# Performance work log

Hardware: AMD Instinct MI355X
Metric: run time of the kernel (lower is better)

## Reference

```python
import jax, jax.numpy as jnp
import numpy as np

HEADS = 12
EMBED = 768
HEAD_DIM = EMBED // HEADS
SCALING = HEAD_DIM ** (-0.5)


def setup_inputs() -> dict:
    key = jax.random.key(0)
    k1, k2, k3, k4, k5 = jax.random.split(key, 5)
    B, N = 8, 1024
    x = jax.random.normal(k1, (B, N, EMBED), dtype=jnp.float32)
    W_qkv = jax.random.normal(k2, (3 * EMBED, EMBED), dtype=jnp.float32) * 0.02
    b_qkv = jax.random.normal(k3, (3 * EMBED,), dtype=jnp.float32) * 0.02
    W_proj = jax.random.normal(k4, (EMBED, EMBED), dtype=jnp.float32) * 0.02
    b_proj = jax.random.normal(k5, (EMBED,), dtype=jnp.float32) * 0.02
    return {"x": x, "W_qkv": W_qkv, "b_qkv": b_qkv, "W_proj": W_proj, "b_proj": b_proj}


def reference(x, W_qkv, b_qkv, W_proj, b_proj):
    B, N, D = x.shape
    # fused QKV projection: [B, N, 3D]
    qkv = x @ W_qkv.T + b_qkv
    # split last dim as (u=3, h, e) per einops 'b n (u h e) -> u b h n e'
    qkv = qkv.reshape(B, N, 3, HEADS, HEAD_DIM).transpose(2, 0, 3, 1, 4)
    q, k, v = qkv[0], qkv[1], qkv[2]
    # raw dot-product scores (NO pre-softmax scaling, per original)
    sim = jnp.einsum('bhqi,bhki->bhqk', q, k)
    # unusual POST-softmax scaling
    sim = jax.nn.softmax(sim, axis=-1) * SCALING
    att = jnp.einsum('bhnk,bhke->bhne', sim, v)
    att = att.transpose(0, 2, 1, 3).reshape(B, N, D)  # b h n e -> b n (h e)
    return att @ W_proj.T + b_proj
```

## Files before the change

### kernel.cpp

```cpp
#include <hip/hip_runtime.h>

typedef unsigned short u16;
typedef __attribute__((ext_vector_type(8))) short bf16x8;
typedef __attribute__((ext_vector_type(4))) float f32x4;

#define HEADS 12
#define HDIM  64
#define EMBED 768
#define TD    2304
#define SEQ   1024
#define MTOK  8192
#define GK    768
#define GNT   12

__device__ __forceinline__ u16 f2bf(float f) {
  union { float f; unsigned u; } x; x.f = f;
  unsigned r = x.u + 0x7fffu + ((x.u >> 16) & 1u);
  return (u16)(r >> 16);
}

__global__ void cast3_kernel(const float* __restrict__ x, const float* __restrict__ wq,
                             const float* __restrict__ wp, u16* __restrict__ xb,
                             u16* __restrict__ wqb, u16* __restrict__ wpb) {
  const int N1 = MTOK * EMBED / 4, N2 = TD * EMBED / 4, N3 = EMBED * EMBED / 4;
  int i = blockIdx.x * blockDim.x + threadIdx.x;
  int st = gridDim.x * blockDim.x;
  for (; i < N1 + N2 + N3; i += st) {
    const float* s; u16* d; int j;
    if (i < N1)           { s = x;  d = xb;  j = i; }
    else if (i < N1 + N2) { s = wq; d = wqb; j = i - N1; }
    else                  { s = wp; d = wpb; j = i - N1 - N2; }
    float4 v = reinterpret_cast<const float4*>(s)[j];
    ushort4 o;
    o.x = f2bf(v.x); o.y = f2bf(v.y); o.z = f2bf(v.z); o.w = f2bf(v.w);
    reinterpret_cast<ushort4*>(d)[j] = o;
  }
}

__device__ __forceinline__ void gload_lds16(const u16* g, u16* l) {
  __builtin_amdgcn_global_load_lds(
      (const __attribute__((address_space(1))) unsigned*)g,
      (__attribute__((address_space(3))) unsigned*)l, 16, 0, 0);
}

__device__ __forceinline__ void memfence_bar() {
  asm volatile("" ::: "memory");
  __builtin_amdgcn_s_barrier();
  asm volatile("" ::: "memory");
}

template <bool OUT_BF16>
__global__ __launch_bounds__(256, 2) void gemm_phase(const u16* __restrict__ A,
                                                     const u16* __restrict__ B,
                                                     const float* __restrict__ bias,
                                                     void* __restrict__ Cv,
                                                     int NBN, int Ndim) {
  __shared__ u16 As[3][128 * 64];
  __shared__ u16 Bs[2][96 * 64];
  const int tid  = threadIdx.x;
  const int wave = tid >> 6, lane = tid & 63;
  const int wr = wave >> 1, wc = wave & 1;
  const int lr = lane & 15, g = lane >> 4;

  const int nwg = gridDim.x;
  const int swz = (blockIdx.x & 7) * (nwg >> 3) + (blockIdx.x >> 3);
  const int ny = swz % NBN, mx = swz / NBN;

  const u16* Ag = A + (size_t)(mx * 128) * GK;
  const u16* Bg = B + (size_t)(ny * 96) * GK;

  const int srow   = lane >> 3;
  const int schunk = (lane & 7) ^ srow;

  auto stageA = [&](int kt, int buf) {
#pragma unroll
    for (int c = 0; c < 4; ++c) {
      int slot = wave * 4 + c;
      int row  = slot * 8 + srow;
      gload_lds16(Ag + (size_t)row * GK + kt * 64 + schunk * 8, &As[buf][slot * 512]);
    }
  };
  auto stageB = [&](int kt, int buf) {
#pragma unroll
    for (int c = 0; c < 3; ++c) {
      int slot = wave * 3 + c;
      int row  = slot * 8 + srow;
      gload_lds16(Bg + (size_t)row * GK + kt * 64 + schunk * 8, &Bs[buf][slot * 512]);
    }
  };

  f32x4 acc[4][3];
#pragma unroll
  for (int m = 0; m < 4; ++m)
#pragma unroll
    for (int n = 0; n < 3; ++n) acc[m][n] = 0.f;

  stageA(0, 0);
  stageB(0, 0);
  stageA(1, 1);
  asm volatile("s_waitcnt vmcnt(4)" ::: "memory");
  memfence_bar();

  int ra = 0, rb = 0;
  for (int t = 0; t < GNT; ++t) {
    bf16x8 af[4][2], bf0[3], bf1[3];
#pragma unroll
    for (int m = 0; m < 4; ++m)
#pragma unroll
      for (int kk = 0; kk < 2; ++kk) {
        int r = wr * 64 + m * 16 + lr;
        af[m][kk] = *reinterpret_cast<const bf16x8*>(
            &As[ra][r * 64 + (((kk * 4 + g) ^ (r & 7)) << 3)]);
      }
#pragma unroll
    for (int n = 0; n < 3; ++n) {
      int r = wc * 48 + n * 16 + lr;
      bf0[n] = *reinterpret_cast<const bf16x8*>(&Bs[rb][r * 64 + ((g ^ (r & 7)) << 3)]);
    }
    if (t + 1 < GNT) stageB(t + 1, rb ^ 1);
    if (t + 2 < GNT) stageA(t + 2, ra >= 1 ? ra - 1 : 2);
    memfence_bar();
    asm volatile("s_waitcnt lgkmcnt(0)" ::: "memory");
    __builtin_amdgcn_sched_barrier(0);
    __builtin_amdgcn_s_setprio(1);
#pragma unroll
    for (int m = 0; m < 4; ++m)
#pragma unroll
      for (int n = 0; n < 3; ++n)
        acc[m][n] = __builtin_amdgcn_mfma_f32_16x16x32_bf16(bf0[n], af[m][0], acc[m][n], 0, 0, 0);
    __builtin_amdgcn_s_setprio(0);

#pragma unroll
    for (int n = 0; n < 3; ++n) {
      int r = wc * 48 + n * 16 + lr;
      bf1[n] = *reinterpret_cast<const bf16x8*>(&Bs[rb][r * 64 + (((4 + g) ^ (r & 7)) << 3)]);
    }
    memfence_bar();
    asm volatile("s_waitcnt lgkmcnt(0)" ::: "memory");
    __builtin_amdgcn_sched_barrier(0);
    __builtin_amdgcn_s_setprio(1);
#pragma unroll
    for (int m = 0; m < 4; ++m)
#pragma unroll
      for (int n = 0; n < 3; ++n)
        acc[m][n] = __builtin_amdgcn_mfma_f32_16x16x32_bf16(bf1[n], af[m][1], acc[m][n], 0, 0, 0);
    __builtin_amdgcn_s_setprio(0);

    if (t < GNT - 2) {
      asm volatile("s_waitcnt vmcnt(4)" ::: "memory");
      memfence_bar();
    } else if (t == GNT - 2) {
      asm volatile("s_waitcnt vmcnt(0)" ::: "memory");
      memfence_bar();
    }
    ra = (ra == 2) ? 0 : ra + 1;
    rb ^= 1;
  }

  const int row0 = mx * 128 + wr * 64 + lr;
  const int col0 = ny * 96 + wc * 48 + g * 4;
#pragma unroll
  for (int m = 0; m < 4; ++m)
#pragma unroll
    for (int n = 0; n < 3; ++n) {
      int row = row0 + m * 16;
      int col = col0 + n * 16;
      float4 bv = *reinterpret_cast<const float4*>(&bias[col]);
      float v0 = acc[m][n][0] + bv.x, v1 = acc[m][n][1] + bv.y;
      float v2 = acc[m][n][2] + bv.z, v3 = acc[m][n][3] + bv.w;
      if (OUT_BF16) {
        ushort4 pw;
        pw.x = f2bf(v0); pw.y = f2bf(v1); pw.z = f2bf(v2); pw.w = f2bf(v3);
        *reinterpret_cast<ushort4*>(&((u16*)Cv)[(size_t)row * Ndim + col]) = pw;
      } else {
        *reinterpret_cast<float4*>(&((float*)Cv)[(size_t)row * Ndim + col]) =
            make_float4(v0, v1, v2, v3);
      }
    }
}

__global__ __launch_bounds__(256) void vtrans_kernel(const u16* __restrict__ qkv,
                                                     u16* __restrict__ vt) {
  const int bh = blockIdx.x, kb = blockIdx.y;
  const int b = bh / HEADS, h = bh % HEADS;
  __shared__ u16 Ls[64 * 72];
  const int t = threadIdx.x;
  const int row = t >> 2, seg = t & 3;
  const u16* src = qkv + (size_t)(b * SEQ + kb * 64 + row) * TD + 2 * EMBED + h * HDIM + seg * 16;
  *reinterpret_cast<uint4*>(&Ls[row * 72 + seg * 16])     = *reinterpret_cast<const uint4*>(src);
  *reinterpret_cast<uint4*>(&Ls[row * 72 + seg * 16 + 8]) = *reinterpret_cast<const uint4*>(src + 8);
  __syncthreads();
  u16 tmp[16];
#pragma unroll
  for (int i = 0; i < 16; ++i) tmp[i] = Ls[(seg * 16 + i) * 72 + row];
  u16* dst = vt + (size_t)bh * (HDIM * SEQ) + (size_t)row * SEQ + kb * 64 + seg * 16;
  *reinterpret_cast<uint4*>(dst)     = *reinterpret_cast<const uint4*>(tmp);
  *reinterpret_cast<uint4*>(dst + 8) = *reinterpret_cast<const uint4*>(tmp + 8);
}

__global__ __launch_bounds__(256, 3) void attn_kernel(const u16* __restrict__ qkv,
                                                      const u16* __restrict__ vt,
                                                      u16* __restrict__ ctx) {
  const int bh = blockIdx.x;
  const int b = bh / HEADS, h = bh % HEADS;
  const int qt = blockIdx.y;
  const int tid = threadIdx.x, wave = tid >> 6, lane = tid & 63;
  const int lr = lane & 15, g = lane >> 4;

  __shared__ u16 Ks[2][64 * 64];
  __shared__ u16 Vs[2][64 * 64];
  __shared__ u16 Ps[128 * 64];

  const size_t tok0 = (size_t)b * SEQ;
  const int q0 = qt * 128;
  const int mbase = wave * 32;

  bf16x8 qf[2][2];
#pragma unroll
  for (int mi = 0; mi < 2; ++mi)
#pragma unroll
    for (int dk = 0; dk < 2; ++dk)
      qf[mi][dk] = *reinterpret_cast<const bf16x8*>(
          qkv + (tok0 + q0 + mbase + mi * 16 + lr) * TD + h * HDIM + dk * 32 + g * 8);

  const int srow = lane >> 3;
  const int schunk = (lane & 7) ^ srow;
  const u16* vbase = vt + (size_t)bh * (HDIM * SEQ);

  auto stage = [&](int kb, int buf) {
#pragma unroll
    for (int c2 = 0; c2 < 2; ++c2) {
      int call = wave * 2 + c2;
      int row  = call * 8 + srow;
      gload_lds16(qkv + (tok0 + kb * 64 + row) * TD + EMBED + h * HDIM + schunk * 8,
                  &Ks[buf][call * 512]);
      gload_lds16(vbase + (size_t)row * SEQ + kb * 64 + schunk * 8,
                  &Vs[buf][call * 512]);
    }
  };

  f32x4 oacc[2][4];
#pragma unroll
  for (int mi = 0; mi < 2; ++mi)
#pragma unroll
    for (int e = 0; e < 4; ++e) oacc[mi][e] = 0.f;
  float psum[2] = {0.f, 0.f};

  stage(0, 0);
  asm volatile("s_waitcnt vmcnt(0)" ::: "memory");
  memfence_bar();

  int cur = 0;
  for (int kb = 0; kb < 16; ++kb) {
    if (kb < 15) stage(kb + 1, cur ^ 1);

    bf16x8 ka[4][2];
#pragma unroll
    for (int n = 0; n < 4; ++n)
#pragma unroll
      for (int dk = 0; dk < 2; ++dk) {
        int r = n * 16 + lr;
        int c = dk * 4 + g;
        ka[n][dk] = *reinterpret_cast<const bf16x8*>(&Ks[cur][r * 64 + ((c ^ (r & 7)) << 3)]);
      }
#pragma unroll
    for (int mi = 0; mi < 2; ++mi) {
      int m = mbase + mi * 16 + lr;
      int pswz = (lr & 7) << 1;
#pragma unroll
      for (int n = 0; n < 4; ++n) {
        f32x4 s = 0.f;
        __builtin_amdgcn_s_setprio(1);
        s = __builtin_amdgcn_mfma_f32_16x16x32_bf16(ka[n][0], qf[mi][0], s, 0, 0, 0);
        s = __builtin_amdgcn_mfma_f32_16x16x32_bf16(ka[n][1], qf[mi][1], s, 0, 0, 0);
        __builtin_amdgcn_s_setprio(0);
        float e0 = __expf(s[0]), e1 = __expf(s[1]);
        float e2 = __expf(s[2]), e3 = __expf(s[3]);
        psum[mi] += (e0 + e1) + (e2 + e3);
        ushort4 pw;
        pw.x = f2bf(e0); pw.y = f2bf(e1); pw.z = f2bf(e2); pw.w = f2bf(e3);
        int gran = n * 4 + g;
        *reinterpret_cast<ushort4*>(&Ps[m * 64 + ((gran ^ pswz) << 2)]) = pw;
      }
    }

    bf16x8 vb2[4][2];
#pragma unroll
    for (int e = 0; e < 4; ++e)
#pragma unroll
      for (int kk = 0; kk < 2; ++kk) {
        int r = e * 16 + lr;
        int c = kk * 4 + g;
        vb2[e][kk] = *reinterpret_cast<const bf16x8*>(&Vs[cur][r * 64 + ((c ^ (r & 7)) << 3)]);
      }
#pragma unroll
    for (int mi = 0; mi < 2; ++mi) {
      bf16x8 pa[2];
#pragma unroll
      for (int kk = 0; kk < 2; ++kk) {
        int r = mbase + mi * 16 + lr;
        int c = kk * 4 + g;
        pa[kk] = *reinterpret_cast<const bf16x8*>(&Ps[r * 64 + ((c ^ (r & 7)) << 3)]);
      }
      __builtin_amdgcn_s_setprio(1);
#pragma unroll
      for (int e = 0; e < 4; ++e) {
        oacc[mi][e] = __builtin_amdgcn_mfma_f32_16x16x32_bf16(pa[0], vb2[e][0], oacc[mi][e], 0, 0, 0);
        oacc[mi][e] = __builtin_amdgcn_mfma_f32_16x16x32_bf16(pa[1], vb2[e][1], oacc[mi][e], 0, 0, 0);
      }
      __builtin_amdgcn_s_setprio(0);
    }

    if (kb < 15) {
      asm volatile("s_waitcnt vmcnt(0)" ::: "memory");
      memfence_bar();
    }
    cur ^= 1;
  }

  float scl[2][4];
#pragma unroll
  for (int mi = 0; mi < 2; ++mi) {
    float v = psum[mi];
    v += __shfl_xor(v, 16);
    v += __shfl_xor(v, 32);
    v = 0.125f / v;
#pragma unroll
    for (int j = 0; j < 4; ++j) scl[mi][j] = __shfl(v, 4 * g + j);
  }
#pragma unroll
  for (int mi = 0; mi < 2; ++mi)
#pragma unroll
    for (int e = 0; e < 4; ++e)
#pragma unroll
      for (int j = 0; j < 4; ++j) {
        float v = oacc[mi][e][j] * scl[mi][j];
        ctx[(tok0 + q0 + mbase + mi * 16 + 4 * g + j) * EMBED + h * HDIM + e * 16 + lr] = f2bf(v);
      }
}

extern "C" void kernel_launch(void* const* d_in, const int* in_sizes, int n_in,
                              void* d_out, int out_size, void* d_ws, size_t ws_size,
                              hipStream_t stream) {
  (void)in_sizes; (void)n_in; (void)out_size;
  const float* x     = (const float*)d_in[0];
  const float* Wqkv  = (const float*)d_in[1];
  const float* bqkv  = (const float*)d_in[2];
  const float* Wproj = (const float*)d_in[3];
  const float* bproj = (const float*)d_in[4];
  float* out = (float*)d_out;

  char* ws = (char*)d_ws;
  size_t off = 0;
  auto alloc = [&](size_t bytes) {
    char* p = ws + off;
    off += (bytes + 255) & ~(size_t)255;
    return p;
  };
  u16* xb     = (u16*)alloc((size_t)MTOK * EMBED * 2);
  u16* wqkvb  = (u16*)alloc((size_t)TD * EMBED * 2);
  u16* wprojb = (u16*)alloc((size_t)EMBED * EMBED * 2);
  u16* qkvb   = (u16*)alloc((size_t)MTOK * TD * 2);
  u16* ctxb   = (u16*)alloc((size_t)MTOK * EMBED * 2);
  if (off > ws_size) return;
  u16* vtb = xb;

  cast3_kernel<<<dim3(2048), dim3(256), 0, stream>>>(x, Wqkv, Wproj, xb, wqkvb, wprojb);

  gemm_phase<true><<<dim3(1536), dim3(256), 0, stream>>>(xb, wqkvb, bqkv, qkvb, 24, TD);
  vtrans_kernel<<<dim3(96, 16), dim3(256), 0, stream>>>(qkvb, vtb);
  attn_kernel<<<dim3(96, 8), dim3(256), 0, stream>>>(qkvb, vtb, ctxb);
  gemm_phase<false><<<dim3(512), dim3(256), 0, stream>>>(ctxb, wprojb, bproj, out, 8, EMBED);
}
```

Measured before the change: 125.1 us.

## Restructure GEMM into triple-buffered K=32 pipeline with register double-buffering

The GEMM kernel now uses a K-step of 32 instead of 64, with triple-buffered LDS tiles for both A and B. Global loads are issued three stages ahead, and fragment reads for the next step are double-buffered in registers so they overlap the current MFMAs. The smaller LDS footprint allows launch bounds of 3 blocks per CU, but the XOR swizzle is dropped, which may bring LDS bank conflicts. In the attention kernel the V fragment loads are hoisted alongside the K loads, which raises register pressure.

Result: slower. 134.3 us (+7.3%).

```diff
diff --git a/kernel.cpp b/kernel.cpp
--- a/kernel.cpp
+++ b/kernel.cpp
@@ -11,7 +11,7 @@
 #define SEQ   1024
 #define MTOK  8192
 #define GK    768
-#define GNT   12
+#define GNT   24
 
 __device__ __forceinline__ u16 f2bf(float f) {
   union { float f; unsigned u; } x; x.f = f;
@@ -50,13 +50,13 @@
 }
 
 template <bool OUT_BF16>
-__global__ __launch_bounds__(256, 2) void gemm_phase(const u16* __restrict__ A,
-                                                     const u16* __restrict__ B,
-                                                     const float* __restrict__ bias,
-                                                     void* __restrict__ Cv,
-                                                     int NBN, int Ndim) {
-  __shared__ u16 As[3][128 * 64];
-  __shared__ u16 Bs[2][96 * 64];
+__global__ __launch_bounds__(256, 3) void gemm_pipe(const u16* __restrict__ A,
+                                                    const u16* __restrict__ B,
+                                                    const float* __restrict__ bias,
+                                                    void* __restrict__ Cv,
+                                                    int NBN, int Ndim) {
+  __shared__ u16 As[3][128 * 32];
+  __shared__ u16 Bs[3][96 * 32];
   const int tid  = threadIdx.x;
   const int wave = tid >> 6, lane = tid & 63;
   const int wr = wave >> 1, wc = wave & 1;
@@ -69,24 +69,38 @@
   const u16* Ag = A + (size_t)(mx * 128) * GK;
   const u16* Bg = B + (size_t)(ny * 96) * GK;
 
-  const int srow   = lane >> 3;
-  const int schunk = (lane & 7) ^ srow;
-
-  auto stageA = [&](int kt, int buf) {
-#pragma unroll
-    for (int c = 0; c < 4; ++c) {
-      int slot = wave * 4 + c;
-      int row  = slot * 8 + srow;
-      gload_lds16(Ag + (size_t)row * GK + kt * 64 + schunk * 8, &As[buf][slot * 512]);
-    }
-  };
-  auto stageB = [&](int kt, int buf) {
-#pragma unroll
-    for (int c = 0; c < 3; ++c) {
-      int slot = wave * 3 + c;
-      int row  = slot * 8 + srow;
-      gload_lds16(Bg + (size_t)row * GK + kt * 64 + schunk * 8, &Bs[buf][slot * 512]);
-    }
+  const int srow = lane >> 2;
+  const int scol = (lane & 3) * 8;
+
+  auto stage = [&](int kt) {
+    const int buf = kt % 3;
+    const int k0 = kt * 32;
+#pragma unroll
+    for (int c = 0; c < 2; ++c) {
+      int slot = wave * 2 + c;
+      int row  = slot * 16 + srow;
+      gload_lds16(Ag + (size_t)row * GK + k0 + scol, &As[buf][slot * 512]);
+    }
+    if (wave < 2) {
+#pragma unroll
+      for (int c = 0; c < 2; ++c) {
+        int slot = wave * 2 + c;
+        int row  = slot * 16 + srow;
+        gload_lds16(Bg + (size_t)row * GK + k0 + scol, &Bs[buf][slot * 512]);
+      }
+    } else {
+      int slot = wave + 2;
+      int row  = slot * 16 + srow;
+      gload_lds16(Bg + (size_t)row * GK + k0 + scol, &Bs[buf][slot * 512]);
+    }
+  };
+  auto vmwait2 = [&] {
+    if (wave < 2) asm volatile("s_waitcnt vmcnt(8)" ::: "memory");
+    else          asm volatile("s_waitcnt vmcnt(6)" ::: "memory");
+  };
+  auto vmwait1 = [&] {
+    if (wave < 2) asm volatile("s_waitcnt vmcnt(4)" ::: "memory");
+    else          asm volatile("s_waitcnt vmcnt(3)" ::: "memory");
   };
 
   f32x4 acc[4][3];
@@ -95,66 +109,46 @@
 #pragma unroll
     for (int n = 0; n < 3; ++n) acc[m][n] = 0.f;
 
-  stageA(0, 0);
-  stageB(0, 0);
-  stageA(1, 1);
-  asm volatile("s_waitcnt vmcnt(4)" ::: "memory");
+  auto readfr = [&](int u, bf16x8* af, bf16x8* bf) {
+    const int buf = u % 3;
+#pragma unroll
+    for (int m = 0; m < 4; ++m)
+      af[m] = *reinterpret_cast<const bf16x8*>(&As[buf][(wr * 64 + m * 16 + lr) * 32 + g * 8]);
+#pragma unroll
+    for (int n = 0; n < 3; ++n)
+      bf[n] = *reinterpret_cast<const bf16x8*>(&Bs[buf][(wc * 48 + n * 16 + lr) * 32 + g * 8]);
+  };
+  auto domfma = [&](const bf16x8* af, const bf16x8* bf) {
+    __builtin_amdgcn_s_setprio(1);
+#pragma unroll
+    for (int m = 0; m < 4; ++m)
+#pragma unroll
+      for (int n = 0; n < 3; ++n)
+        acc[m][n] = __builtin_amdgcn_mfma_f32_16x16x32_bf16(bf[n], af[m], acc[m][n], 0, 0, 0);
+    __builtin_amdgcn_s_setprio(0);
+  };
+  auto halfiter = [&](int u, const bf16x8* afc, const bf16x8* bfc,
+                      bf16x8* afn, bf16x8* bfn) {
+    asm volatile("s_waitcnt lgkmcnt(0)" ::: "memory");
+    memfence_bar();
+    if (u + 3 < GNT) stage(u + 3);
+    if (u + 3 < GNT)      vmwait2();
+    else if (u + 3 == GNT) vmwait1();
+    else if (u + 2 == GNT) asm volatile("s_waitcnt vmcnt(0)" ::: "memory");
+    if (u + 1 < GNT) readfr(u + 1, afn, bfn);
+    domfma(afc, bfc);
+  };
+
+  bf16x8 af0[4], bf0[3], af1[4], bf1[3];
+
+  stage(0); stage(1); stage(2);
+  vmwait2();
   memfence_bar();
-
-  int ra = 0, rb = 0;
-  for (int t = 0; t < GNT; ++t) {
-    bf16x8 af[4][2], bf0[3], bf1[3];
-#pragma unroll
-    for (int m = 0; m < 4; ++m)
-#pragma unroll
-      for (int kk = 0; kk < 2; ++kk) {
-        int r = wr * 64 + m * 16 + lr;
-        af[m][kk] = *reinterpret_cast<const bf16x8*>(
-            &As[ra][r * 64 + (((kk * 4 + g) ^ (r & 7)) << 3)]);
-      }
-#pragma unroll
-    for (int n = 0; n < 3; ++n) {
-      int r = wc * 48 + n * 16 + lr;
-      bf0[n] = *reinterpret_cast<const bf16x8*>(&Bs[rb][r * 64 + ((g ^ (r & 7)) << 3)]);
-    }
-    if (t + 1 < GNT) stageB(t + 1, rb ^ 1);
-    if (t + 2 < GNT) stageA(t + 2, ra >= 1 ? ra - 1 : 2);
-    memfence_bar();
-    asm volatile("s_waitcnt lgkmcnt(0)" ::: "memory");
-    __builtin_amdgcn_sched_barrier(0);
-    __builtin_amdgcn_s_setprio(1);
-#pragma unroll
-    for (int m = 0; m < 4; ++m)
-#pragma unroll
-      for (int n = 0; n < 3; ++n)
-        acc[m][n] = __builtin_amdgcn_mfma_f32_16x16x32_bf16(bf0[n], af[m][0], acc[m][n], 0, 0, 0);
-    __builtin_amdgcn_s_setprio(0);
-
-#pragma unroll
-    for (int n = 0; n < 3; ++n) {
-      int r = wc * 48 + n * 16 + lr;
-      bf1[n] = *reinterpret_cast<const bf16x8*>(&Bs[rb][r * 64 + (((4 + g) ^ (r & 7)) << 3)]);
-    }
-    memfence_bar();
-    asm volatile("s_waitcnt lgkmcnt(0)" ::: "memory");
-    __builtin_amdgcn_sched_barrier(0);
-    __builtin_amdgcn_s_setprio(1);
-#pragma unroll
-    for (int m = 0; m < 4; ++m)
-#pragma unroll
-      for (int n = 0; n < 3; ++n)
-        acc[m][n] = __builtin_amdgcn_mfma_f32_16x16x32_bf16(bf1[n], af[m][1], acc[m][n], 0, 0, 0);
-    __builtin_amdgcn_s_setprio(0);
-
-    if (t < GNT - 2) {
-      asm volatile("s_waitcnt vmcnt(4)" ::: "memory");
-      memfence_bar();
-    } else if (t == GNT - 2) {
-      asm volatile("s_waitcnt vmcnt(0)" ::: "memory");
-      memfence_bar();
-    }
-    ra = (ra == 2) ? 0 : ra + 1;
-    rb ^= 1;
+  readfr(0, af0, bf0);
+
+  for (int t = 0; t < GNT; t += 2) {
+    halfiter(t,     af0, bf0, af1, bf1);
+    halfiter(t + 1, af1, bf1, af0, bf0);
   }
 
   const int row0 = mx * 128 + wr * 64 + lr;
@@ -254,15 +248,17 @@
   for (int kb = 0; kb < 16; ++kb) {
     if (kb < 15) stage(kb + 1, cur ^ 1);
 
-    bf16x8 ka[4][2];
+    bf16x8 ka[4][2], vb2[4][2];
 #pragma unroll
     for (int n = 0; n < 4; ++n)
 #pragma unroll
       for (int dk = 0; dk < 2; ++dk) {
         int r = n * 16 + lr;
         int c = dk * 4 + g;
-        ka[n][dk] = *reinterpret_cast<const bf16x8*>(&Ks[cur][r * 64 + ((c ^ (r & 7)) << 3)]);
-      }
+        ka[n][dk]  = *reinterpret_cast<const bf16x8*>(&Ks[cur][r * 64 + ((c ^ (r & 7)) << 3)]);
+        vb2[n][dk] = *reinterpret_cast<const bf16x8*>(&Vs[cur][r * 64 + ((c ^ (r & 7)) << 3)]);
+      }
+
 #pragma unroll
     for (int mi = 0; mi < 2; ++mi) {
       int m = mbase + mi * 16 + lr;
@@ -284,15 +280,6 @@
       }
     }
 
-    bf16x8 vb2[4][2];
-#pragma unroll
-    for (int e = 0; e < 4; ++e)
-#pragma unroll
-      for (int kk = 0; kk < 2; ++kk) {
-        int r = e * 16 + lr;
-        int c = kk * 4 + g;
-        vb2[e][kk] = *reinterpret_cast<const bf16x8*>(&Vs[cur][r * 64 + ((c ^ (r & 7)) << 3)]);
-      }
 #pragma unroll
     for (int mi = 0; mi < 2; ++mi) {
       bf16x8 pa[2];
@@ -367,8 +354,8 @@
 
   cast3_kernel<<<dim3(2048), dim3(256), 0, stream>>>(x, Wqkv, Wproj, xb, wqkvb, wprojb);
 
-  gemm_phase<true><<<dim3(1536), dim3(256), 0, stream>>>(xb, wqkvb, bqkv, qkvb, 24, TD);
+  gemm_pipe<true><<<dim3(1536), dim3(256), 0, stream>>>(xb, wqkvb, bqkv, qkvb, 24, TD);
   vtrans_kernel<<<dim3(96, 16), dim3(256), 0, stream>>>(qkvb, vtb);
   attn_kernel<<<dim3(96, 8), dim3(256), 0, stream>>>(qkvb, vtb, ctxb);
-  gemm_phase<false><<<dim3(512), dim3(256), 0, stream>>>(ctxb, wprojb, bproj, out, 8, EMBED);
-}
+  gemm_pipe<false><<<dim3(512), dim3(256), 0, stream>>>(ctxb, wprojb, bproj, out, 8, EMBED);
+}
```
